# Kernel tuning notes

Measured on AMD Instinct MI355X. Metric: run time of the kernel, lower is better.

The kernel has to match this reference:

```python
import jax, jax.numpy as jnp
import numpy as np

EPS = 1e-6
DROP_RATE = 0.25

def setup_inputs() -> dict:
    key = jax.random.key(0)
    k1, k2, k3 = jax.random.split(key, 3)
    B, S, D = 4, 2048, 2048
    inputs = jax.random.normal(k1, (B, S, D), dtype=jnp.float32)
    # keras 'uniform' initializer: U(-0.05, 0.05)
    W_1 = jax.random.uniform(k2, (D, D), dtype=jnp.float32, minval=-0.05, maxval=0.05)
    W_2 = jax.random.uniform(k3, (D, D), dtype=jnp.float32, minval=-0.05, maxval=0.05)
    return {"inputs": inputs, "W_1": W_1, "W_2": W_2}

def reference(inputs, W_1, W_2):
    # LayerNorm over last axis (no affine: gamma/beta unused in original call)
    mean = jnp.mean(inputs, axis=-1, keepdims=True)
    var = jnp.mean(jnp.square(inputs - mean), axis=-1, keepdims=True)
    x_norm = (inputs - mean) / jnp.sqrt(var + EPS)          # [B,S,D]
    # 2-layer MLP with relu
    h = jax.nn.relu(jnp.einsum('bsd,de->bse', x_norm, W_1))  # [B,S,D]
    y = jnp.einsum('bsd,de->bse', h, W_2)                    # [B,S,D]
    # dropout(0.25), inverted scaling, fixed key for determinism
    keep = jax.random.bernoulli(jax.random.key(1), 1.0 - DROP_RATE, y.shape)
    y_drop = jnp.where(keep, y / (1.0 - DROP_RATE), 0.0)
    return x_norm + y_drop
```

## Files before the change

### kernel.cpp

```cpp
#include <hip/hip_runtime.h>
#include <hip/hip_bf16.h>
#include <stdint.h>

#define M_DIM 8192
#define N_DIM 2048
#define K_DIM 2048

typedef __bf16 bf16x8_t __attribute__((ext_vector_type(8)));
typedef float f32x4_t __attribute__((ext_vector_type(4)));

__device__ __forceinline__ unsigned tf_rotl(unsigned x, int r) {
  return (x << r) | (x >> (32 - r));
}
__device__ __forceinline__ unsigned threefry_mask_bits(unsigned ctr) {
  unsigned x0 = 0u, x1 = ctr;
  const unsigned ks0 = 0u, ks1 = 1u, ks2 = 0x1BD11BDBu;
  x0 += ks0; x1 += ks1;
#define TFR(r) { x0 += x1; x1 = tf_rotl(x1, (r)); x1 ^= x0; }
  TFR(13) TFR(15) TFR(26) TFR(6)
  x0 += ks1; x1 += ks2 + 1u;
  TFR(17) TFR(29) TFR(16) TFR(24)
  x0 += ks2; x1 += ks0 + 2u;
  TFR(13) TFR(15) TFR(26) TFR(6)
  x0 += ks0; x1 += ks1 + 3u;
  TFR(17) TFR(29) TFR(16) TFR(24)
  x0 += ks1; x1 += ks2 + 4u;
  TFR(13) TFR(15) TFR(26) TFR(6)
  x0 += ks2; x1 += ks0 + 5u;
#undef TFR
  return x0 ^ x1;
}

__device__ __forceinline__ void gload_lds16(const __hip_bfloat16* g, unsigned short* l) {
  __builtin_amdgcn_global_load_lds(
      (const __attribute__((address_space(1))) unsigned int*)g,
      (__attribute__((address_space(3))) unsigned int*)l,
      16, 0, 0);
}

__global__ __launch_bounds__(256) void wt_kernel(
    const float* __restrict__ W1, const float* __restrict__ W2,
    __hip_bfloat16* __restrict__ W1t, __hip_bfloat16* __restrict__ W2t) {
  __shared__ float tile[32][33];
  const float* src = blockIdx.z ? W2 : W1;
  __hip_bfloat16* dst = blockIdx.z ? W2t : W1t;
  int x = blockIdx.x * 32 + threadIdx.x;
  int y = blockIdx.y * 32 + threadIdx.y;
#pragma unroll
  for (int i = 0; i < 32; i += 8)
    tile[threadIdx.y + i][threadIdx.x] = src[(size_t)(y + i) * N_DIM + x];
  __syncthreads();
  int xo = blockIdx.y * 32 + threadIdx.x;
  int yo = blockIdx.x * 32 + threadIdx.y;
#pragma unroll
  for (int i = 0; i < 32; i += 8)
    dst[(size_t)(yo + i) * K_DIM + xo] = __float2bfloat16(tile[threadIdx.x][threadIdx.y + i]);
}

__global__ __launch_bounds__(256) void ln_kernel(const float* __restrict__ X,
                                                 __hip_bfloat16* __restrict__ Xn) {
  const int row = blockIdx.x;
  const float4* xv = (const float4*)(X + (size_t)row * K_DIM);
  float4 v0 = xv[threadIdx.x];
  float4 v1 = xv[threadIdx.x + 256];
  float s  = v0.x + v0.y + v0.z + v0.w + v1.x + v1.y + v1.z + v1.w;
  float ss = v0.x*v0.x + v0.y*v0.y + v0.z*v0.z + v0.w*v0.w
           + v1.x*v1.x + v1.y*v1.y + v1.z*v1.z + v1.w*v1.w;
#pragma unroll
  for (int off = 32; off > 0; off >>= 1) {
    s  += __shfl_xor(s, off);
    ss += __shfl_xor(ss, off);
  }
  __shared__ float rs[4], rss[4];
  const int wave = threadIdx.x >> 6;
  if ((threadIdx.x & 63) == 0) { rs[wave] = s; rss[wave] = ss; }
  __syncthreads();
  float S  = rs[0] + rs[1] + rs[2] + rs[3];
  float SS = rss[0] + rss[1] + rss[2] + rss[3];
  float mean = S * (1.0f / 2048.0f);
  float var  = SS * (1.0f / 2048.0f) - mean * mean;
  float rstd = 1.0f / sqrtf(var + 1e-6f);
  float vv[8] = {v0.x, v0.y, v0.z, v0.w, v1.x, v1.y, v1.z, v1.w};
  unsigned short o[8];
#pragma unroll
  for (int i = 0; i < 8; i++) {
    __hip_bfloat16 b = __float2bfloat16((vv[i] - mean) * rstd);
    o[i] = *(unsigned short*)&b;
  }
  ushort4* dst = (ushort4*)(Xn + (size_t)row * K_DIM);
  dst[threadIdx.x]       = make_ushort4(o[0], o[1], o[2], o[3]);
  dst[threadIdx.x + 256] = make_ushort4(o[4], o[5], o[6], o[7]);
}

template <int EPI>
__global__ __launch_bounds__(256) void gemm128(
    const __hip_bfloat16* __restrict__ A,
    const __hip_bfloat16* __restrict__ Bt,
    const __hip_bfloat16* __restrict__ Xn,
    __hip_bfloat16* __restrict__ Hout,
    float* __restrict__ Fout) {
  __shared__ unsigned short As[2][128 * 64];
  __shared__ unsigned short Bs[2][128 * 64];
  const int tid  = threadIdx.x;
  const int lane = tid & 63;
  const int wave = tid >> 6;
  const int wm = wave >> 1, wn = wave & 1;
  const int mBase = blockIdx.x * 128;
  const int nBase = blockIdx.y * 128;

  f32x4_t acc[4][4];
#pragma unroll
  for (int i = 0; i < 4; i++)
#pragma unroll
    for (int j = 0; j < 4; j++) acc[i][j] = (f32x4_t){0.f, 0.f, 0.f, 0.f};

  const int rowIn  = lane >> 3;
  const int csrc   = ((lane & 7) ^ (rowIn & 7)) << 3;
  const __hip_bfloat16* aSrc[4];
  const __hip_bfloat16* bSrc[4];
  int sDst[4];
#pragma unroll
  for (int j = 0; j < 4; j++) {
    const int ca = wave + 4 * j;
    aSrc[j] = A  + (size_t)(mBase + 8 * ca + rowIn) * K_DIM + csrc;
    bSrc[j] = Bt + (size_t)(nBase + 8 * ca + rowIn) * K_DIM + csrc;
    sDst[j] = ca * 512;
  }

  const int fr = lane & 15;
  const int fq = lane >> 4;
  const int sw = fr & 7;
  const int cA0 = (fq ^ sw) * 8;
  const int cA1 = ((4 | fq) ^ sw) * 8;
  const int rowOffA = (wm * 64 + fr) * 64;
  const int rowOffB = (wn * 64 + fr) * 64;

#define STAGE(buf, k0)                                        \
  {                                                           \
    _Pragma("unroll")                                         \
    for (int j = 0; j < 4; j++) {                             \
      gload_lds16(aSrc[j] + (k0), &As[buf][sDst[j]]);         \
      gload_lds16(bSrc[j] + (k0), &Bs[buf][sDst[j]]);         \
    }                                                         \
  }

#define COMPUTE_HALF(buf, cOff)                                                 \
  {                                                                             \
    bf16x8_t af[4], bfr[4];                                                     \
    _Pragma("unroll")                                                           \
    for (int i = 0; i < 4; i++) af[i]  = *(const bf16x8_t*)(&As[buf][rowOffA + i * 1024 + (cOff)]); \
    _Pragma("unroll")                                                           \
    for (int i = 0; i < 4; i++) bfr[i] = *(const bf16x8_t*)(&Bs[buf][rowOffB + i * 1024 + (cOff)]); \
    _Pragma("unroll")                                                           \
    for (int mi = 0; mi < 4; mi++)                                              \
      _Pragma("unroll")                                                         \
      for (int ni = 0; ni < 4; ni++)                                            \
        acc[mi][ni] = __builtin_amdgcn_mfma_f32_16x16x32_bf16(af[mi], bfr[ni], acc[mi][ni], 0, 0, 0); \
  }
#define COMPUTE(buf) { COMPUTE_HALF(buf, cA0) COMPUTE_HALF(buf, cA1) }

  STAGE(0, 0)
  for (int k0 = 0; k0 < K_DIM - 128; k0 += 128) {
    __syncthreads();
    STAGE(1, k0 + 64)
    COMPUTE(0)
    __syncthreads();
    STAGE(0, k0 + 128)
    COMPUTE(1)
  }
  __syncthreads();
  STAGE(1, K_DIM - 64)
  COMPUTE(0)
  __syncthreads();
  COMPUTE(1)
#undef STAGE
#undef COMPUTE
#undef COMPUTE_HALF

  const int mRow = mBase + wm * 64;
  const int nCol = nBase + wn * 64;
#pragma unroll
  for (int mi = 0; mi < 4; mi++) {
#pragma unroll
    for (int ni = 0; ni < 4; ni++) {
      const int n  = nCol + ni * 16 + fr;
      const int m0 = mRow + mi * 16 + fq * 4;
#pragma unroll
      for (int r = 0; r < 4; r++) {
        float v = acc[mi][ni][r];
        size_t j = (size_t)(m0 + r) * N_DIM + n;
        if (EPI == 0) {
          Hout[j] = __float2bfloat16(fmaxf(v, 0.0f));
        } else {
          unsigned bits = threefry_mask_bits((unsigned)j);
          float y  = (bits < 0xC0000000u) ? v * (1.0f / 0.75f) : 0.0f;
          Fout[j]  = __bfloat162float(Xn[j]) + y;
        }
      }
    }
  }
}

extern "C" void kernel_launch(void* const* d_in, const int* in_sizes, int n_in,
                              void* d_out, int out_size, void* d_ws, size_t ws_size,
                              hipStream_t stream) {
  (void)in_sizes; (void)n_in; (void)out_size; (void)ws_size;
  const float* X  = (const float*)d_in[0];
  const float* W1 = (const float*)d_in[1];
  const float* W2 = (const float*)d_in[2];
  float* out = (float*)d_out;

  unsigned char* ws = (unsigned char*)d_ws;
  __hip_bfloat16* Xn  = (__hip_bfloat16*)(ws);
  __hip_bfloat16* H   = (__hip_bfloat16*)(ws + ((size_t)32 << 20));
  __hip_bfloat16* W1t = (__hip_bfloat16*)(ws + ((size_t)64 << 20));
  __hip_bfloat16* W2t = (__hip_bfloat16*)(ws + ((size_t)72 << 20));

  wt_kernel<<<dim3(64, 64, 2), dim3(32, 8, 1), 0, stream>>>(W1, W2, W1t, W2t);
  ln_kernel<<<M_DIM, 256, 0, stream>>>(X, Xn);
  gemm128<0><<<dim3(M_DIM / 128, N_DIM / 128), 256, 0, stream>>>(Xn, W1t, nullptr, H, nullptr);
  gemm128<1><<<dim3(M_DIM / 128, N_DIM / 128), 256, 0, stream>>>(H, W2t, Xn, nullptr, out);
}
```

Measured before the change: 319.8 us.

## Load A fragments directly from global into registers, staging only B in LDS

The A operand no longer goes through shared memory. Each wave loads its own A fragments straight from global memory into double-buffered registers, and only B is staged in LDS through global_load_lds. This halves LDS footprint and LDS read traffic, and launch bounds now request two blocks per CU. In exchange, A rows are read uncoalesced with 16-byte per-lane strided loads, and the two waves sharing the same rows duplicate those reads from global/L2. The extra A registers may also increase register pressure.

```diff
diff --git a/kernel.cpp b/kernel.cpp
--- a/kernel.cpp
+++ b/kernel.cpp
@@ -93,13 +93,12 @@
 }
 
 template <int EPI>
-__global__ __launch_bounds__(256) void gemm128(
+__global__ __launch_bounds__(256, 2) void gemm128(
     const __hip_bfloat16* __restrict__ A,
     const __hip_bfloat16* __restrict__ Bt,
     const __hip_bfloat16* __restrict__ Xn,
     __hip_bfloat16* __restrict__ Hout,
     float* __restrict__ Fout) {
-  __shared__ unsigned short As[2][128 * 64];
   __shared__ unsigned short Bs[2][128 * 64];
   const int tid  = threadIdx.x;
   const int lane = tid & 63;
@@ -114,15 +113,13 @@
 #pragma unroll
     for (int j = 0; j < 4; j++) acc[i][j] = (f32x4_t){0.f, 0.f, 0.f, 0.f};
 
-  const int rowIn  = lane >> 3;
-  const int csrc   = ((lane & 7) ^ (rowIn & 7)) << 3;
-  const __hip_bfloat16* aSrc[4];
+  const int rowIn = lane >> 3;
+  const int csrc  = ((lane & 7) ^ (rowIn & 7)) << 3;
   const __hip_bfloat16* bSrc[4];
   int sDst[4];
 #pragma unroll
   for (int j = 0; j < 4; j++) {
     const int ca = wave + 4 * j;
-    aSrc[j] = A  + (size_t)(mBase + 8 * ca + rowIn) * K_DIM + csrc;
     bSrc[j] = Bt + (size_t)(nBase + 8 * ca + rowIn) * K_DIM + csrc;
     sDst[j] = ca * 512;
   }
@@ -130,52 +127,70 @@
   const int fr = lane & 15;
   const int fq = lane >> 4;
   const int sw = fr & 7;
-  const int cA0 = (fq ^ sw) * 8;
-  const int cA1 = ((4 | fq) ^ sw) * 8;
-  const int rowOffA = (wm * 64 + fr) * 64;
+  const int cB0 = (fq ^ sw) * 8;
+  const int cB1 = ((4 | fq) ^ sw) * 8;
   const int rowOffB = (wn * 64 + fr) * 64;
-
-#define STAGE(buf, k0)                                        \
+  const __hip_bfloat16* aPtr = A + (size_t)(mBase + wm * 64 + fr) * K_DIM + fq * 8;
+
+  bf16x8_t aR0[8], aR1[8];
+
+#define STAGE_B(buf, k0)                                      \
   {                                                           \
     _Pragma("unroll")                                         \
-    for (int j = 0; j < 4; j++) {                             \
-      gload_lds16(aSrc[j] + (k0), &As[buf][sDst[j]]);         \
+    for (int j = 0; j < 4; j++)                               \
       gload_lds16(bSrc[j] + (k0), &Bs[buf][sDst[j]]);         \
-    }                                                         \
-  }
-
-#define COMPUTE_HALF(buf, cOff)                                                 \
+  }
+
+#define LOAD_A(dst, k0)                                                         \
   {                                                                             \
-    bf16x8_t af[4], bfr[4];                                                     \
-    _Pragma("unroll")                                                           \
-    for (int i = 0; i < 4; i++) af[i]  = *(const bf16x8_t*)(&As[buf][rowOffA + i * 1024 + (cOff)]); \
-    _Pragma("unroll")                                                           \
-    for (int i = 0; i < 4; i++) bfr[i] = *(const bf16x8_t*)(&Bs[buf][rowOffB + i * 1024 + (cOff)]); \
+    _Pragma("unroll")                                                           \
+    for (int mi = 0; mi < 4; mi++)                                              \
+      _Pragma("unroll")                                                         \
+      for (int kk = 0; kk < 2; kk++)                                            \
+        dst[mi * 2 + kk] =                                                      \
+            *(const bf16x8_t*)(aPtr + (size_t)mi * 16 * K_DIM + (k0) + kk * 32);\
+  }
+
+#define COMPUTE(buf, aR)                                                        \
+  {                                                                             \
+    bf16x8_t bfr[4];                                                            \
+    _Pragma("unroll")                                                           \
+    for (int ni = 0; ni < 4; ni++) bfr[ni] = *(const bf16x8_t*)(&Bs[buf][rowOffB + ni * 1024 + cB0]); \
     _Pragma("unroll")                                                           \
     for (int mi = 0; mi < 4; mi++)                                              \
       _Pragma("unroll")                                                         \
       for (int ni = 0; ni < 4; ni++)                                            \
-        acc[mi][ni] = __builtin_amdgcn_mfma_f32_16x16x32_bf16(af[mi], bfr[ni], acc[mi][ni], 0, 0, 0); \
-  }
-#define COMPUTE(buf) { COMPUTE_HALF(buf, cA0) COMPUTE_HALF(buf, cA1) }
-
-  STAGE(0, 0)
+        acc[mi][ni] = __builtin_amdgcn_mfma_f32_16x16x32_bf16(aR[mi * 2], bfr[ni], acc[mi][ni], 0, 0, 0); \
+    _Pragma("unroll")                                                           \
+    for (int ni = 0; ni < 4; ni++) bfr[ni] = *(const bf16x8_t*)(&Bs[buf][rowOffB + ni * 1024 + cB1]); \
+    _Pragma("unroll")                                                           \
+    for (int mi = 0; mi < 4; mi++)                                              \
+      _Pragma("unroll")                                                         \
+      for (int ni = 0; ni < 4; ni++)                                            \
+        acc[mi][ni] = __builtin_amdgcn_mfma_f32_16x16x32_bf16(aR[mi * 2 + 1], bfr[ni], acc[mi][ni], 0, 0, 0); \
+  }
+
+  LOAD_A(aR0, 0)
+  STAGE_B(0, 0)
   for (int k0 = 0; k0 < K_DIM - 128; k0 += 128) {
     __syncthreads();
-    STAGE(1, k0 + 64)
-    COMPUTE(0)
+    STAGE_B(1, k0 + 64)
+    LOAD_A(aR1, k0 + 64)
+    COMPUTE(0, aR0)
     __syncthreads();
-    STAGE(0, k0 + 128)
-    COMPUTE(1)
-  }
-  __syncthreads();
-  STAGE(1, K_DIM - 64)
-  COMPUTE(0)
-  __syncthreads();
-  COMPUTE(1)
-#undef STAGE
+    STAGE_B(0, k0 + 128)
+    LOAD_A(aR0, k0 + 128)
+    COMPUTE(1, aR1)
+  }
+  __syncthreads();
+  STAGE_B(1, K_DIM - 64)
+  LOAD_A(aR1, K_DIM - 64)
+  COMPUTE(0, aR0)
+  __syncthreads();
+  COMPUTE(1, aR1)
+#undef STAGE_B
+#undef LOAD_A
 #undef COMPUTE
-#undef COMPUTE_HALF
 
   const int mRow = mBase + wm * 64;
   const int nCol = nBase + wn * 64;
```

Measured after the change: 441.8 us. 1.38x slower.
